# Kernel optimization log

Measured on AMD Instinct MI355X. Metric: run time of the kernel, lower is better.

## Reference

```python
import jax, jax.numpy as jnp
import numpy as np

EMB = 1024
HEADS = 16
HEAD_SZ = EMB // HEADS
EPS = 1e-5


def _layernorm(x, g, b):
    mu = jnp.mean(x, axis=-1, keepdims=True)
    var = jnp.mean(jnp.square(x - mu), axis=-1, keepdims=True)
    return (x - mu) * jax.lax.rsqrt(var + EPS) * g + b


def setup_inputs() -> dict:
    key = jax.random.key(0)
    ks = jax.random.split(key, 12)
    s_in = 1.0 / np.sqrt(EMB)
    s_h = 1.0 / np.sqrt(4 * EMB)
    return {
        "x": jax.random.normal(ks[0], (4, 1024, EMB), jnp.float32),
        # per-head Q/K/V projections stacked: [H, EMB, HEAD_SZ], no bias
        "wq": jax.random.normal(ks[1], (HEADS, EMB, HEAD_SZ), jnp.float32) * s_in,
        "wk": jax.random.normal(ks[2], (HEADS, EMB, HEAD_SZ), jnp.float32) * s_in,
        "wv": jax.random.normal(ks[3], (HEADS, EMB, HEAD_SZ), jnp.float32) * s_in,
        "w_proj": jax.random.normal(ks[4], (EMB, EMB), jnp.float32) * s_in,
        "b_proj": jnp.zeros((EMB,), jnp.float32),
        "w1": jax.random.normal(ks[5], (EMB, 4 * EMB), jnp.float32) * s_in,
        "b1": jnp.zeros((4 * EMB,), jnp.float32),
        "w2": jax.random.normal(ks[6], (4 * EMB, EMB), jnp.float32) * s_h,
        "b2": jnp.zeros((EMB,), jnp.float32),
        "g1": jnp.ones((EMB,), jnp.float32),
        "be1": jnp.zeros((EMB,), jnp.float32),
        "g2": jnp.ones((EMB,), jnp.float32),
        "be2": jnp.zeros((EMB,), jnp.float32),
    }


def reference(x, wq, wk, wv, w_proj, b_proj, w1, b1, w2, b2, g1, be1, g2, be2):
    B, T, C = x.shape
    # --- self-attention (pre-norm) ---
    h = _layernorm(x, g1, be1)
    q = jnp.einsum("btc,hcd->bhtd", h, wq)
    k = jnp.einsum("btc,hcd->bhtd", h, wk)
    v = jnp.einsum("btc,hcd->bhtd", h, wv)
    scale = 1.0 / jnp.sqrt(jnp.asarray(HEAD_SZ, x.dtype))
    scores = jnp.einsum("bhtd,bhsd->bhts", q, k) * scale  # non-causal: SDPA called with no mask
    attn = jax.nn.softmax(scores, axis=-1)
    o = jnp.einsum("bhts,bhsd->bhtd", attn, v)
    o = o.transpose(0, 2, 1, 3).reshape(B, T, C)  # concat heads (same order as torch.cat)
    sa_out = o @ w_proj + b_proj
    x = x + sa_out
    # --- feed-forward; note ln2 applied twice, faithful to source ---
    t = _layernorm(x, g2, be2)
    t = _layernorm(t, g2, be2)
    ff = jax.nn.relu(t @ w1 + b1) @ w2 + b2
    return x + ff
```

## Files before the change

### kernel.cpp

```cpp
#include <hip/hip_runtime.h>
#include <hip/hip_bf16.h>
#include <math.h>
#include <stdint.h>

typedef __bf16 bf16_t;
typedef __bf16 bf16x4 __attribute__((ext_vector_type(4)));
typedef __bf16 bf16x8 __attribute__((ext_vector_type(8)));
typedef float floatx4 __attribute__((ext_vector_type(4)));

#define BM 128
#define BK 32

__device__ __forceinline__ size_t ftaddr(int m, int k, int KT) {
    return ((size_t)(m >> 4) * KT + (k >> 5)) * 512
         + (((k >> 3) & 3) * 16 + (m & 15)) * 8 + (k & 7);
}

__device__ __forceinline__ void gload16(const void* g, void* lds) {
    __builtin_amdgcn_global_load_lds(
        (__attribute__((address_space(1))) void*)(uintptr_t)g,
        (__attribute__((address_space(3))) void*)(uintptr_t)lds,
        16, 0, 0);
}

__global__ void transpose_all(const float* __restrict__ wq, const float* __restrict__ wk,
                              const float* __restrict__ wv, const float* __restrict__ w_proj,
                              const float* __restrict__ w1, const float* __restrict__ w2,
                              bf16_t* __restrict__ WQKVT, bf16_t* __restrict__ WPROJT,
                              bf16_t* __restrict__ W1T, bf16_t* __restrict__ W2T)
{
    const int idx = blockIdx.x;
    const float* in; bf16_t* out; int R, C, rt, ct; long nrow0;
    if (idx < 768) {
        const int z = idx >> 8;
        const int hd = (idx >> 4) & 15;
        rt = idx & 15; ct = 0; R = 1024; C = 64;
        in  = (z == 0 ? wq : z == 1 ? wk : wv) + hd * 65536;
        out = WQKVT; nrow0 = z * 1024 + hd * 64;
    } else if (idx < 1024) {
        const int t = idx - 768; rt = t & 15; ct = t >> 4; R = 1024; C = 1024;
        in = w_proj; out = WPROJT; nrow0 = 0;
    } else if (idx < 2048) {
        const int t = idx - 1024; rt = t & 15; ct = t >> 4; R = 1024; C = 4096;
        in = w1; out = W1T; nrow0 = 0;
    } else {
        const int t = idx - 2048; rt = t & 63; ct = t >> 6; R = 4096; C = 1024;
        in = w2; out = W2T; nrow0 = 0;
    }
    __shared__ float tile[64][65];
    const int tid = threadIdx.x;
    const int r0 = rt * 64, c0 = ct * 64;
    const int tr = tid >> 4;
    const int tc = (tid & 15) * 4;
#pragma unroll
    for (int rr = 0; rr < 4; rr++) {
        const int r = tr + rr * 16;
        const float4 v = *(const float4*)&in[(long)(r0 + r) * C + c0 + tc];
        tile[r][tc + 0] = v.x; tile[r][tc + 1] = v.y;
        tile[r][tc + 2] = v.z; tile[r][tc + 3] = v.w;
    }
    __syncthreads();
    const int KT = R >> 5;
    const int w = tid >> 6, l = tid & 63;
    const int c = l >> 4, rr = l & 15;
#pragma unroll
    for (int it = 0; it < 2; ++it) {
        const int t8 = it * 4 + w;
        const int kt = t8 >> 2;
        const int nb = t8 & 3;
        const long n = nrow0 + c0 + nb * 16 + rr;
        const int k = r0 + kt * 32 + c * 8;
        bf16x8 o;
#pragma unroll
        for (int e = 0; e < 8; e++)
            o[e] = (bf16_t)tile[kt * 32 + c * 8 + e][nb * 16 + rr];
        *(bf16x8*)&out[ftaddr((int)n, k, KT)] = o;
    }
}

__global__ void ln_kernel(const float* __restrict__ x, const float* __restrict__ g,
                          const float* __restrict__ b, bf16_t* __restrict__ outb)
{
    __shared__ __align__(16) bf16_t ybuf[16][1032];
    const int tid = threadIdx.x, wave = tid >> 6, lane = tid & 63;
    const int rb = blockIdx.x;
    float4 gvv[4], bvv[4];
#pragma unroll
    for (int j = 0; j < 4; j++) {
        gvv[j] = ((const float4*)g)[lane + j * 64];
        bvv[j] = ((const float4*)b)[lane + j * 64];
    }
    for (int rr = 0; rr < 4; ++rr) {
        const int lrow = wave * 4 + rr;
        const float* xr = x + (size_t)(rb * 16 + lrow) * 1024;
        float4 v[4];
        float s = 0.f, s2 = 0.f;
#pragma unroll
        for (int j = 0; j < 4; j++) {
            v[j] = ((const float4*)xr)[lane + j * 64];
            s  += v[j].x + v[j].y + v[j].z + v[j].w;
            s2 += v[j].x * v[j].x + v[j].y * v[j].y + v[j].z * v[j].z + v[j].w * v[j].w;
        }
#pragma unroll
        for (int off = 32; off >= 1; off >>= 1) {
            s  += __shfl_xor(s, off);
            s2 += __shfl_xor(s2, off);
        }
        const float mu = s * (1.0f / 1024.0f);
        const float rs = rsqrtf(fmaxf(s2 * (1.0f / 1024.0f) - mu * mu, 0.f) + 1e-5f);
#pragma unroll
        for (int j = 0; j < 4; j++) {
            bf16x4 o;
            o[0] = (bf16_t)((v[j].x - mu) * rs * gvv[j].x + bvv[j].x);
            o[1] = (bf16_t)((v[j].y - mu) * rs * gvv[j].y + bvv[j].y);
            o[2] = (bf16_t)((v[j].z - mu) * rs * gvv[j].z + bvv[j].z);
            o[3] = (bf16_t)((v[j].w - mu) * rs * gvv[j].w + bvv[j].w);
            *(bf16x4*)&ybuf[lrow][(lane + j * 64) * 4] = o;
        }
    }
    __syncthreads();
    bf16_t* outBase = outb + (size_t)rb * 32 * 512;
    for (int it = 0; it < 8; ++it) {
        const int s = it * 256 + tid;
        const int kt = s >> 6, c = (s >> 4) & 3, rr = s & 15;
        const bf16x8 val = *(const bf16x8*)&ybuf[rr][kt * 32 + c * 8];
        *(bf16x8*)&outBase[(size_t)s * 8] = val;
    }
}

__global__ void ln2x_kernel(const float* __restrict__ x, const float* __restrict__ g,
                            const float* __restrict__ b, bf16_t* __restrict__ outb)
{
    __shared__ __align__(16) bf16_t ybuf[16][1032];
    const int tid = threadIdx.x, wave = tid >> 6, lane = tid & 63;
    const int rb = blockIdx.x;
    float4 gvv[4], bvv[4];
#pragma unroll
    for (int j = 0; j < 4; j++) {
        gvv[j] = ((const float4*)g)[lane + j * 64];
        bvv[j] = ((const float4*)b)[lane + j * 64];
    }
    for (int rr = 0; rr < 4; ++rr) {
        const int lrow = wave * 4 + rr;
        const float* xr = x + (size_t)(rb * 16 + lrow) * 1024;
        float4 v[4];
        float s = 0.f, s2 = 0.f;
#pragma unroll
        for (int j = 0; j < 4; j++) {
            v[j] = ((const float4*)xr)[lane + j * 64];
            s  += v[j].x + v[j].y + v[j].z + v[j].w;
            s2 += v[j].x * v[j].x + v[j].y * v[j].y + v[j].z * v[j].z + v[j].w * v[j].w;
        }
#pragma unroll
        for (int off = 32; off >= 1; off >>= 1) {
            s  += __shfl_xor(s, off);
            s2 += __shfl_xor(s2, off);
        }
        float mu = s * (1.0f / 1024.0f);
        float rs = rsqrtf(fmaxf(s2 * (1.0f / 1024.0f) - mu * mu, 0.f) + 1e-5f);
        s = 0.f; s2 = 0.f;
#pragma unroll
        for (int j = 0; j < 4; j++) {
            v[j].x = (v[j].x - mu) * rs * gvv[j].x + bvv[j].x;
            v[j].y = (v[j].y - mu) * rs * gvv[j].y + bvv[j].y;
            v[j].z = (v[j].z - mu) * rs * gvv[j].z + bvv[j].z;
            v[j].w = (v[j].w - mu) * rs * gvv[j].w + bvv[j].w;
            s  += v[j].x + v[j].y + v[j].z + v[j].w;
            s2 += v[j].x * v[j].x + v[j].y * v[j].y + v[j].z * v[j].z + v[j].w * v[j].w;
        }
#pragma unroll
        for (int off = 32; off >= 1; off >>= 1) {
            s  += __shfl_xor(s, off);
            s2 += __shfl_xor(s2, off);
        }
        mu = s * (1.0f / 1024.0f);
        rs = rsqrtf(fmaxf(s2 * (1.0f / 1024.0f) - mu * mu, 0.f) + 1e-5f);
#pragma unroll
        for (int j = 0; j < 4; j++) {
            bf16x4 o;
            o[0] = (bf16_t)((v[j].x - mu) * rs * gvv[j].x + bvv[j].x);
            o[1] = (bf16_t)((v[j].y - mu) * rs * gvv[j].y + bvv[j].y);
            o[2] = (bf16_t)((v[j].z - mu) * rs * gvv[j].z + bvv[j].z);
            o[3] = (bf16_t)((v[j].w - mu) * rs * gvv[j].w + bvv[j].w);
            *(bf16x4*)&ybuf[lrow][(lane + j * 64) * 4] = o;
        }
    }
    __syncthreads();
    bf16_t* outBase = outb + (size_t)rb * 32 * 512;
    for (int it = 0; it < 8; ++it) {
        const int s = it * 256 + tid;
        const int kt = s >> 6, c = (s >> 4) & 3, rr = s & 15;
        const bf16x8 val = *(const bf16x8*)&ybuf[rr][kt * 32 + c * 8];
        *(bf16x8*)&outBase[(size_t)s * 8] = val;
    }
}

template<int EPI, int BNt>
__global__ __launch_bounds__(256, 2)
void gemm_bt(const bf16_t* __restrict__ A, const bf16_t* __restrict__ Bt,
             const int K,
             const float* __restrict__ bias, const float* __restrict__ resid,
             float* __restrict__ outf, bf16_t* __restrict__ outb,
             bf16_t* __restrict__ aux1, bf16_t* __restrict__ aux2,
             const int Nout)
{
    constexpr int NFRAG = BNt / 16;
    __shared__ __align__(16) bf16_t As[3][8 * 512];
    __shared__ __align__(16) bf16_t Bs[3][NFRAG * 512];
    const int tid  = threadIdx.x;
    const int wave = tid >> 6, lane = tid & 63;
    const int bm = blockIdx.x * BM, bn = blockIdx.y * BNt;
    const int KT = K >> 5;

    floatx4 acc[2][NFRAG];
#pragma unroll
    for (int i = 0; i < 2; i++)
#pragma unroll
        for (int j = 0; j < NFRAG; j++) acc[i][j] = (floatx4){0.f, 0.f, 0.f, 0.f};

    const bf16_t* gA0 = A + ((size_t)(bm / 16 + wave * 2 + 0) * KT) * 512 + lane * 8;
    const bf16_t* gA1 = A + ((size_t)(bm / 16 + wave * 2 + 1) * KT) * 512 + lane * 8;
    const int lA0 = (wave * 2 + 0) * 512;
    const int lA1 = (wave * 2 + 1) * 512;

    const bf16_t* gB0;
    const bf16_t* gB1 = nullptr;
    int lB0, lB1 = 0;
    if (BNt == 128) {
        gB0 = Bt + ((size_t)(bn / 16 + wave * 2 + 0) * KT) * 512 + lane * 8;
        gB1 = Bt + ((size_t)(bn / 16 + wave * 2 + 1) * KT) * 512 + lane * 8;
        lB0 = (wave * 2 + 0) * 512;
        lB1 = (wave * 2 + 1) * 512;
    } else {
        gB0 = Bt + ((size_t)(bn / 16 + wave) * KT) * 512 + lane * 8;
        lB0 = wave * 512;
    }

    auto stage = [&](int t, int bu) {
        const size_t off = (size_t)t * 512;
        gload16(gA0 + off, (bf16_t*)As[bu] + lA0);
        gload16(gA1 + off, (bf16_t*)As[bu] + lA1);
        gload16(gB0 + off, (bf16_t*)Bs[bu] + lB0);
        if (BNt == 128) gload16(gB1 + off, (bf16_t*)Bs[bu] + lB1);
    };

    auto compute = [&](int bu) {
        bf16x8 af[2], bfv[NFRAG];
#pragma unroll
        for (int i = 0; i < 2; i++)
            af[i] = *(const bf16x8*)&As[bu][(wave * 2 + i) * 512 + lane * 8];
#pragma unroll
        for (int j = 0; j < NFRAG; j++)
            bfv[j] = *(const bf16x8*)&Bs[bu][j * 512 + lane * 8];
#pragma unroll
        for (int i = 0; i < 2; i++)
#pragma unroll
            for (int j = 0; j < NFRAG; j++)
                acc[i][j] = __builtin_amdgcn_mfma_f32_16x16x32_bf16(af[i], bfv[j], acc[i][j], 0, 0, 0);
    };

    const int NT = K / BK;
    stage(0, 0);
    stage(1, 1);
    int bu = 0;
    for (int t = 0; t < NT - 1; ++t) {
        if (BNt == 128) asm volatile("s_waitcnt vmcnt(4)\n\ts_barrier" ::: "memory");
        else            asm volatile("s_waitcnt vmcnt(3)\n\ts_barrier" ::: "memory");
        if (t + 2 < NT) stage(t + 2, (t + 2) % 3);
        compute(bu);
        bu = (bu + 1) % 3;
    }
    asm volatile("s_waitcnt vmcnt(0)\n\ts_barrier" ::: "memory");
    compute(bu);

    const int er = (lane >> 4) * 4, ec = lane & 15;
#pragma unroll
    for (int i = 0; i < 2; i++) {
#pragma unroll
        for (int j = 0; j < NFRAG; j++) {
            const int col = bn + j * 16 + ec;
#pragma unroll
            for (int r = 0; r < 4; r++) {
                const int row = bm + wave * 32 + i * 16 + er + r;
                const float v = acc[i][j][r];
                if (EPI == 0) {
                    const int b = row >> 10, t = row & 1023;
                    if (col < 1024) {
                        const int h = col >> 6, d = col & 63;
                        outb[(size_t)((b * 16 + h) * 1024 + t) * 64 + d] = (bf16_t)v;
                    } else if (col < 2048) {
                        const int c2 = col - 1024, h = c2 >> 6, d = c2 & 63;
                        aux1[(size_t)((b * 16 + h) * 1024 + t) * 64 + d] = (bf16_t)v;
                    } else {
                        const int c2 = col - 2048, h = c2 >> 6, d = c2 & 63;
                        aux2[(size_t)((b * 16 + h) * 64 + d) * 1024 + t] = (bf16_t)v;
                    }
                } else if (EPI == 1 || EPI == 3) {
                    const size_t idx = (size_t)row * Nout + col;
                    outf[idx] = v + bias[col] + resid[idx];
                } else if (EPI == 2) {
                    outb[ftaddr(row, col, Nout >> 5)] = (bf16_t)fmaxf(v + bias[col], 0.f);
                }
            }
        }
    }
}

__global__ __launch_bounds__(256, 4)
void attn_kernel(const bf16_t* __restrict__ Q, const bf16_t* __restrict__ Kg,
                 const bf16_t* __restrict__ Vt, bf16_t* __restrict__ Og)
{
    __shared__ __align__(16) bf16_t Ks[2][4096];
    __shared__ __align__(16) bf16_t Vs[2][4096];
    __shared__ __align__(16) bf16_t Ps[4][1024];
    const int tid = threadIdx.x, wave = tid >> 6, lane = tid & 63;
    const int bh = blockIdx.y;
    const int b = bh >> 4, h = bh & 15;
    const int q0 = blockIdx.x * 64 + wave * 16;
    const bf16_t* Qb = Q + (size_t)bh * 65536;
    const char* Kb = (const char*)(Kg + (size_t)bh * 65536);
    const char* Vb = (const char*)(Vt + (size_t)bh * 65536);
    const int fr = lane & 15, g = lane >> 4, fk = g * 8;

    const bf16x8 qf0 = *(const bf16x8*)&Qb[(size_t)(q0 + fr) * 64 + fk];
    const bf16x8 qf1 = *(const bf16x8*)&Qb[(size_t)(q0 + fr) * 64 + 32 + fk];

    floatx4 o[4];
#pragma unroll
    for (int dt = 0; dt < 4; dt++) o[dt] = (floatx4){0.f, 0.f, 0.f, 0.f};
    float lsum[4] = {0.f, 0.f, 0.f, 0.f};
    bf16_t* pw = &Ps[wave][0];
    const float sscale = 0.125f * 1.44269504088896f;

    auto stage = [&](int s0, int bu) {
#pragma unroll
        for (int t = 0; t < 2; t++) {
            const int j = wave * 2 + t;
            gload16(Kb + (size_t)(s0 + lane) * 128 + j * 16, &Ks[bu][j * 512]);
            gload16(Vb + (size_t)lane * 2048 + (size_t)s0 * 2 + j * 16, &Vs[bu][j * 512]);
        }
    };

    stage(0, 0);
    int bu = 0;
    for (int it = 0; it < 16; ++it) {
        __syncthreads();
        if (it < 15) stage((it + 1) * 64, bu ^ 1);
        const bf16_t* Kl = Ks[bu];
        const bf16_t* Vl = Vs[bu];

        floatx4 sacc[4];
#pragma unroll
        for (int ss = 0; ss < 4; ss++) sacc[ss] = (floatx4){0.f, 0.f, 0.f, 0.f};
#pragma unroll
        for (int c = 0; c < 2; c++) {
            const int ch = c * 4 + g;
            const bf16x8 qf = (c == 0) ? qf0 : qf1;
#pragma unroll
            for (int ss = 0; ss < 4; ss++) {
                const bf16x8 kf = *(const bf16x8*)&Kl[ch * 512 + (ss * 16 + fr) * 8];
                sacc[ss] = __builtin_amdgcn_mfma_f32_16x16x32_bf16(qf, kf, sacc[ss], 0, 0, 0);
            }
        }
#pragma unroll
        for (int ss = 0; ss < 4; ss++) {
#pragma unroll
            for (int r = 0; r < 4; r++) {
                const float p = __builtin_amdgcn_exp2f(sacc[ss][r] * sscale);
                lsum[r] += p;
                const int q = g * 4 + r;
                pw[(ss * 2 + (fr >> 3)) * 128 + q * 8 + (fr & 7)] = (bf16_t)p;
            }
        }
        asm volatile("s_waitcnt lgkmcnt(0)" ::: "memory");
#pragma unroll
        for (int c = 0; c < 2; c++) {
            const int ch = c * 4 + g;
            const bf16x8 pf = *(const bf16x8*)&pw[ch * 128 + fr * 8];
#pragma unroll
            for (int dt = 0; dt < 4; dt++) {
                const bf16x8 vf = *(const bf16x8*)&Vl[ch * 512 + (dt * 16 + fr) * 8];
                o[dt] = __builtin_amdgcn_mfma_f32_16x16x32_bf16(pf, vf, o[dt], 0, 0, 0);
            }
        }
        asm volatile("" ::: "memory");
        bu ^= 1;
    }
#pragma unroll
    for (int r = 0; r < 4; r++) {
        float l = lsum[r];
        l += __shfl_xor(l, 1);
        l += __shfl_xor(l, 2);
        l += __shfl_xor(l, 4);
        l += __shfl_xor(l, 8);
        lsum[r] = 1.0f / l;
    }
    const int tq = q0 + g * 4;
#pragma unroll
    for (int dt = 0; dt < 4; dt++) {
#pragma unroll
        for (int r = 0; r < 4; r++) {
            const int m = b * 1024 + tq + r;
            const int k = h * 64 + dt * 16 + fr;
            Og[ftaddr(m, k, 32)] = (bf16_t)(o[dt][r] * lsum[r]);
        }
    }
}

extern "C" void kernel_launch(void* const* d_in, const int* in_sizes, int n_in,
                              void* d_out, int out_size, void* d_ws, size_t ws_size,
                              hipStream_t stream)
{
    const float* x      = (const float*)d_in[0];
    const float* wq     = (const float*)d_in[1];
    const float* wk     = (const float*)d_in[2];
    const float* wv     = (const float*)d_in[3];
    const float* w_proj = (const float*)d_in[4];
    const float* b_proj = (const float*)d_in[5];
    const float* w1     = (const float*)d_in[6];
    const float* b1     = (const float*)d_in[7];
    const float* w2     = (const float*)d_in[8];
    const float* b2     = (const float*)d_in[9];
    const float* g1     = (const float*)d_in[10];
    const float* be1    = (const float*)d_in[11];
    const float* g2     = (const float*)d_in[12];
    const float* be2    = (const float*)d_in[13];
    float* out = (float*)d_out;
    char* ws = (char*)d_ws;

    bf16_t* WQKVT = (bf16_t*)(ws + 0x0000000);
    bf16_t* WPROJT= (bf16_t*)(ws + 0x0600000);
    bf16_t* W1T   = (bf16_t*)(ws + 0x0800000);
    bf16_t* W2T   = (bf16_t*)(ws + 0x1000000);
    bf16_t* HB    = (bf16_t*)(ws + 0x1800000);
    bf16_t* Qb    = (bf16_t*)(ws + 0x2000000);
    bf16_t* Kb    = (bf16_t*)(ws + 0x2800000);
    bf16_t* Vtb   = (bf16_t*)(ws + 0x3000000);
    bf16_t* AO    = (bf16_t*)(ws + 0x3800000);
    float*  X2    = (float*)(ws + 0x4000000);
    bf16_t* TB    = (bf16_t*)(ws + 0x2800000);
    bf16_t* FF1B  = (bf16_t*)(ws + 0x5000000);

    dim3 blk(256);
    transpose_all<<<3072, blk, 0, stream>>>(wq, wk, wv, w_proj, w1, w2,
                                            WQKVT, WPROJT, W1T, W2T);
    ln_kernel<<<256, blk, 0, stream>>>(x, g1, be1, HB);
    gemm_bt<0, 128><<<dim3(32, 24), blk, 0, stream>>>(HB, WQKVT, 1024, nullptr, nullptr,
                                                      nullptr, Qb, Kb, Vtb, 3072);
    attn_kernel<<<dim3(16, 64), blk, 0, stream>>>(Qb, Kb, Vtb, AO);
    gemm_bt<1, 64><<<dim3(32, 16), blk, 0, stream>>>(AO, WPROJT, 1024, b_proj, x,
                                                     X2, nullptr, nullptr, nullptr, 1024);
    ln2x_kernel<<<256, blk, 0, stream>>>(X2, g2, be2, TB);
    gemm_bt<2, 128><<<dim3(32, 32), blk, 0, stream>>>(TB, W1T, 1024, b1, nullptr,
                                                      nullptr, FF1B, nullptr, nullptr, 4096);
    gemm_bt<3, 64><<<dim3(32, 16), blk, 0, stream>>>(FF1B, W2T, 4096, b2, X2,
                                                     out, nullptr, nullptr, nullptr, 1024);
}
```

Measured before the change: 316.8 us.

## Merge weight transpose with LN1 and stage V-transpose epilogue through LDS

```diff
diff --git a/kernel.cpp b/kernel.cpp
--- a/kernel.cpp
+++ b/kernel.cpp
@@ -23,63 +23,116 @@
         16, 0, 0);
 }
 
-__global__ void transpose_all(const float* __restrict__ wq, const float* __restrict__ wk,
-                              const float* __restrict__ wv, const float* __restrict__ w_proj,
-                              const float* __restrict__ w1, const float* __restrict__ w2,
-                              bf16_t* __restrict__ WQKVT, bf16_t* __restrict__ WPROJT,
-                              bf16_t* __restrict__ W1T, bf16_t* __restrict__ W2T)
+__global__ void prep_kernel(const float* __restrict__ wq, const float* __restrict__ wk,
+                            const float* __restrict__ wv, const float* __restrict__ w_proj,
+                            const float* __restrict__ w1, const float* __restrict__ w2,
+                            bf16_t* __restrict__ WQKVT, bf16_t* __restrict__ WPROJT,
+                            bf16_t* __restrict__ W1T, bf16_t* __restrict__ W2T,
+                            const float* __restrict__ x, const float* __restrict__ g1,
+                            const float* __restrict__ be1, bf16_t* __restrict__ HB)
 {
-    const int idx = blockIdx.x;
-    const float* in; bf16_t* out; int R, C, rt, ct; long nrow0;
-    if (idx < 768) {
-        const int z = idx >> 8;
-        const int hd = (idx >> 4) & 15;
-        rt = idx & 15; ct = 0; R = 1024; C = 64;
-        in  = (z == 0 ? wq : z == 1 ? wk : wv) + hd * 65536;
-        out = WQKVT; nrow0 = z * 1024 + hd * 64;
-    } else if (idx < 1024) {
-        const int t = idx - 768; rt = t & 15; ct = t >> 4; R = 1024; C = 1024;
-        in = w_proj; out = WPROJT; nrow0 = 0;
-    } else if (idx < 2048) {
-        const int t = idx - 1024; rt = t & 15; ct = t >> 4; R = 1024; C = 4096;
-        in = w1; out = W1T; nrow0 = 0;
+    __shared__ __align__(16) char psm[33024];
+    const int tid = threadIdx.x;
+    if (blockIdx.x < 3072) {
+        float (*tile)[65] = (float(*)[65])psm;
+        const int idx = blockIdx.x;
+        const float* in; bf16_t* out; int R, C, rt, ct; long nrow0;
+        if (idx < 768) {
+            const int z = idx >> 8;
+            const int hd = (idx >> 4) & 15;
+            rt = idx & 15; ct = 0; R = 1024; C = 64;
+            in  = (z == 0 ? wq : z == 1 ? wk : wv) + hd * 65536;
+            out = WQKVT; nrow0 = z * 1024 + hd * 64;
+        } else if (idx < 1024) {
+            const int t = idx - 768; rt = t & 15; ct = t >> 4; R = 1024; C = 1024;
+            in = w_proj; out = WPROJT; nrow0 = 0;
+        } else if (idx < 2048) {
+            const int t = idx - 1024; rt = t & 15; ct = t >> 4; R = 1024; C = 4096;
+            in = w1; out = W1T; nrow0 = 0;
+        } else {
+            const int t = idx - 2048; rt = t & 63; ct = t >> 6; R = 4096; C = 1024;
+            in = w2; out = W2T; nrow0 = 0;
+        }
+        const int r0 = rt * 64, c0 = ct * 64;
+        const int tr = tid >> 4;
+        const int tc = (tid & 15) * 4;
+#pragma unroll
+        for (int rr = 0; rr < 4; rr++) {
+            const int r = tr + rr * 16;
+            const float4 v = *(const float4*)&in[(long)(r0 + r) * C + c0 + tc];
+            tile[r][tc + 0] = v.x; tile[r][tc + 1] = v.y;
+            tile[r][tc + 2] = v.z; tile[r][tc + 3] = v.w;
+        }
+        __syncthreads();
+        const int KT = R >> 5;
+        const int w = tid >> 6, l = tid & 63;
+        const int c = l >> 4, rr2 = l & 15;
+#pragma unroll
+        for (int it = 0; it < 2; ++it) {
+            const int t8 = it * 4 + w;
+            const int kt = t8 >> 2;
+            const int nb = t8 & 3;
+            const long n = nrow0 + c0 + nb * 16 + rr2;
+            const int k = r0 + kt * 32 + c * 8;
+            bf16x8 o;
+#pragma unroll
+            for (int e = 0; e < 8; e++)
+                o[e] = (bf16_t)tile[kt * 32 + c * 8 + e][nb * 16 + rr2];
+            *(bf16x8*)&out[ftaddr((int)n, k, KT)] = o;
+        }
     } else {
-        const int t = idx - 2048; rt = t & 63; ct = t >> 6; R = 4096; C = 1024;
-        in = w2; out = W2T; nrow0 = 0;
-    }
-    __shared__ float tile[64][65];
-    const int tid = threadIdx.x;
-    const int r0 = rt * 64, c0 = ct * 64;
-    const int tr = tid >> 4;
-    const int tc = (tid & 15) * 4;
-#pragma unroll
-    for (int rr = 0; rr < 4; rr++) {
-        const int r = tr + rr * 16;
-        const float4 v = *(const float4*)&in[(long)(r0 + r) * C + c0 + tc];
-        tile[r][tc + 0] = v.x; tile[r][tc + 1] = v.y;
-        tile[r][tc + 2] = v.z; tile[r][tc + 3] = v.w;
-    }
-    __syncthreads();
-    const int KT = R >> 5;
-    const int w = tid >> 6, l = tid & 63;
-    const int c = l >> 4, rr = l & 15;
-#pragma unroll
-    for (int it = 0; it < 2; ++it) {
-        const int t8 = it * 4 + w;
-        const int kt = t8 >> 2;
-        const int nb = t8 & 3;
-        const long n = nrow0 + c0 + nb * 16 + rr;
-        const int k = r0 + kt * 32 + c * 8;
-        bf16x8 o;
-#pragma unroll
-        for (int e = 0; e < 8; e++)
-            o[e] = (bf16_t)tile[kt * 32 + c * 8 + e][nb * 16 + rr];
-        *(bf16x8*)&out[ftaddr((int)n, k, KT)] = o;
-    }
-}
-
-__global__ void ln_kernel(const float* __restrict__ x, const float* __restrict__ g,
-                          const float* __restrict__ b, bf16_t* __restrict__ outb)
+        bf16_t (*ybuf)[1032] = (bf16_t(*)[1032])psm;
+        const int wave = tid >> 6, lane = tid & 63;
+        const int rb = blockIdx.x - 3072;
+        float4 gvv[4], bvv[4];
+#pragma unroll
+        for (int j = 0; j < 4; j++) {
+            gvv[j] = ((const float4*)g1)[lane + j * 64];
+            bvv[j] = ((const float4*)be1)[lane + j * 64];
+        }
+#pragma unroll
+        for (int rr = 0; rr < 4; ++rr) {
+            const int lrow = wave * 4 + rr;
+            const float* xr = x + (size_t)(rb * 16 + lrow) * 1024;
+            float4 v[4];
+            float s = 0.f, s2 = 0.f;
+#pragma unroll
+            for (int j = 0; j < 4; j++) {
+                v[j] = ((const float4*)xr)[lane + j * 64];
+                s  += v[j].x + v[j].y + v[j].z + v[j].w;
+                s2 += v[j].x * v[j].x + v[j].y * v[j].y + v[j].z * v[j].z + v[j].w * v[j].w;
+            }
+#pragma unroll
+            for (int off = 32; off >= 1; off >>= 1) {
+                s  += __shfl_xor(s, off);
+                s2 += __shfl_xor(s2, off);
+            }
+            const float mu = s * (1.0f / 1024.0f);
+            const float rs = rsqrtf(fmaxf(s2 * (1.0f / 1024.0f) - mu * mu, 0.f) + 1e-5f);
+#pragma unroll
+            for (int j = 0; j < 4; j++) {
+                bf16x4 o;
+                o[0] = (bf16_t)((v[j].x - mu) * rs * gvv[j].x + bvv[j].x);
+                o[1] = (bf16_t)((v[j].y - mu) * rs * gvv[j].y + bvv[j].y);
+                o[2] = (bf16_t)((v[j].z - mu) * rs * gvv[j].z + bvv[j].z);
+                o[3] = (bf16_t)((v[j].w - mu) * rs * gvv[j].w + bvv[j].w);
+                *(bf16x4*)&ybuf[lrow][(lane + j * 64) * 4] = o;
+            }
+        }
+        __syncthreads();
+        bf16_t* outBase = HB + (size_t)rb * 32 * 512;
+#pragma unroll
+        for (int it = 0; it < 8; ++it) {
+            const int s = it * 256 + tid;
+            const int kt = s >> 6, c = (s >> 4) & 3, rr2 = s & 15;
+            const bf16x8 val = *(const bf16x8*)&ybuf[rr2][kt * 32 + c * 8];
+            *(bf16x8*)&outBase[(size_t)s * 8] = val;
+        }
+    }
+}
+
+__global__ void ln2x_kernel(const float* __restrict__ x, const float* __restrict__ g,
+                            const float* __restrict__ b, bf16_t* __restrict__ outb)
 {
     __shared__ __align__(16) bf16_t ybuf[16][1032];
     const int tid = threadIdx.x, wave = tid >> 6, lane = tid & 63;
@@ -90,6 +143,7 @@
         gvv[j] = ((const float4*)g)[lane + j * 64];
         bvv[j] = ((const float4*)b)[lane + j * 64];
     }
+#pragma unroll
     for (int rr = 0; rr < 4; ++rr) {
         const int lrow = wave * 4 + rr;
         const float* xr = x + (size_t)(rb * 16 + lrow) * 1024;
@@ -106,8 +160,25 @@
             s  += __shfl_xor(s, off);
             s2 += __shfl_xor(s2, off);
         }
-        const float mu = s * (1.0f / 1024.0f);
-        const float rs = rsqrtf(fmaxf(s2 * (1.0f / 1024.0f) - mu * mu, 0.f) + 1e-5f);
+        float mu = s * (1.0f / 1024.0f);
+        float rs = rsqrtf(fmaxf(s2 * (1.0f / 1024.0f) - mu * mu, 0.f) + 1e-5f);
+        s = 0.f; s2 = 0.f;
+#pragma unroll
+        for (int j = 0; j < 4; j++) {
+            v[j].x = (v[j].x - mu) * rs * gvv[j].x + bvv[j].x;
+            v[j].y = (v[j].y - mu) * rs * gvv[j].y + bvv[j].y;
+            v[j].z = (v[j].z - mu) * rs * gvv[j].z + bvv[j].z;
+            v[j].w = (v[j].w - mu) * rs * gvv[j].w + bvv[j].w;
+            s  += v[j].x + v[j].y + v[j].z + v[j].w;
+            s2 += v[j].x * v[j].x + v[j].y * v[j].y + v[j].z * v[j].z + v[j].w * v[j].w;
+        }
+#pragma unroll
+        for (int off = 32; off >= 1; off >>= 1) {
+            s  += __shfl_xor(s, off);
+            s2 += __shfl_xor(s2, off);
+        }
+        mu = s * (1.0f / 1024.0f);
+        rs = rsqrtf(fmaxf(s2 * (1.0f / 1024.0f) - mu * mu, 0.f) + 1e-5f);
 #pragma unroll
         for (int j = 0; j < 4; j++) {
             bf16x4 o;
@@ -120,77 +191,11 @@
     }
     __syncthreads();
     bf16_t* outBase = outb + (size_t)rb * 32 * 512;
+#pragma unroll
     for (int it = 0; it < 8; ++it) {
         const int s = it * 256 + tid;
-        const int kt = s >> 6, c = (s >> 4) & 3, rr = s & 15;
-        const bf16x8 val = *(const bf16x8*)&ybuf[rr][kt * 32 + c * 8];
-        *(bf16x8*)&outBase[(size_t)s * 8] = val;
-    }
-}
-
-__global__ void ln2x_kernel(const float* __restrict__ x, const float* __restrict__ g,
-                            const float* __restrict__ b, bf16_t* __restrict__ outb)
-{
-    __shared__ __align__(16) bf16_t ybuf[16][1032];
-    const int tid = threadIdx.x, wave = tid >> 6, lane = tid & 63;
-    const int rb = blockIdx.x;
-    float4 gvv[4], bvv[4];
-#pragma unroll
-    for (int j = 0; j < 4; j++) {
-        gvv[j] = ((const float4*)g)[lane + j * 64];
-        bvv[j] = ((const float4*)b)[lane + j * 64];
-    }
-    for (int rr = 0; rr < 4; ++rr) {
-        const int lrow = wave * 4 + rr;
-        const float* xr = x + (size_t)(rb * 16 + lrow) * 1024;
-        float4 v[4];
-        float s = 0.f, s2 = 0.f;
-#pragma unroll
-        for (int j = 0; j < 4; j++) {
-            v[j] = ((const float4*)xr)[lane + j * 64];
-            s  += v[j].x + v[j].y + v[j].z + v[j].w;
-            s2 += v[j].x * v[j].x + v[j].y * v[j].y + v[j].z * v[j].z + v[j].w * v[j].w;
-        }
-#pragma unroll
-        for (int off = 32; off >= 1; off >>= 1) {
-            s  += __shfl_xor(s, off);
-            s2 += __shfl_xor(s2, off);
-        }
-        float mu = s * (1.0f / 1024.0f);
-        float rs = rsqrtf(fmaxf(s2 * (1.0f / 1024.0f) - mu * mu, 0.f) + 1e-5f);
-        s = 0.f; s2 = 0.f;
-#pragma unroll
-        for (int j = 0; j < 4; j++) {
-            v[j].x = (v[j].x - mu) * rs * gvv[j].x + bvv[j].x;
-            v[j].y = (v[j].y - mu) * rs * gvv[j].y + bvv[j].y;
-            v[j].z = (v[j].z - mu) * rs * gvv[j].z + bvv[j].z;
-            v[j].w = (v[j].w - mu) * rs * gvv[j].w + bvv[j].w;
-            s  += v[j].x + v[j].y + v[j].z + v[j].w;
-            s2 += v[j].x * v[j].x + v[j].y * v[j].y + v[j].z * v[j].z + v[j].w * v[j].w;
-        }
-#pragma unroll
-        for (int off = 32; off >= 1; off >>= 1) {
-            s  += __shfl_xor(s, off);
-            s2 += __shfl_xor(s2, off);
-        }
-        mu = s * (1.0f / 1024.0f);
-        rs = rsqrtf(fmaxf(s2 * (1.0f / 1024.0f) - mu * mu, 0.f) + 1e-5f);
-#pragma unroll
-        for (int j = 0; j < 4; j++) {
-            bf16x4 o;
-            o[0] = (bf16_t)((v[j].x - mu) * rs * gvv[j].x + bvv[j].x);
-            o[1] = (bf16_t)((v[j].y - mu) * rs * gvv[j].y + bvv[j].y);
-            o[2] = (bf16_t)((v[j].z - mu) * rs * gvv[j].z + bvv[j].z);
-            o[3] = (bf16_t)((v[j].w - mu) * rs * gvv[j].w + bvv[j].w);
-            *(bf16x4*)&ybuf[lrow][(lane + j * 64) * 4] = o;
-        }
-    }
-    __syncthreads();
-    bf16_t* outBase = outb + (size_t)rb * 32 * 512;
-    for (int it = 0; it < 8; ++it) {
-        const int s = it * 256 + tid;
-        const int kt = s >> 6, c = (s >> 4) & 3, rr = s & 15;
-        const bf16x8 val = *(const bf16x8*)&ybuf[rr][kt * 32 + c * 8];
+        const int kt = s >> 6, c = (s >> 4) & 3, rr2 = s & 15;
+        const bf16x8 val = *(const bf16x8*)&ybuf[rr2][kt * 32 + c * 8];
         *(bf16x8*)&outBase[(size_t)s * 8] = val;
     }
 }
@@ -205,8 +210,11 @@
              const int Nout)
 {
     constexpr int NFRAG = BNt / 16;
-    __shared__ __align__(16) bf16_t As[3][8 * 512];
-    __shared__ __align__(16) bf16_t Bs[3][NFRAG * 512];
+    constexpr int ASZ = 3 * 8 * 512;
+    constexpr int BSZ = 3 * NFRAG * 512;
+    __shared__ __align__(16) bf16_t smem[ASZ + BSZ];
+    bf16_t* Asb = smem;
+    bf16_t* Bsb = smem + ASZ;
     const int tid  = threadIdx.x;
     const int wave = tid >> 6, lane = tid & 63;
     const int bm = blockIdx.x * BM, bn = blockIdx.y * BNt;
@@ -238,20 +246,20 @@
 
     auto stage = [&](int t, int bu) {
         const size_t off = (size_t)t * 512;
-        gload16(gA0 + off, (bf16_t*)As[bu] + lA0);
-        gload16(gA1 + off, (bf16_t*)As[bu] + lA1);
-        gload16(gB0 + off, (bf16_t*)Bs[bu] + lB0);
-        if (BNt == 128) gload16(gB1 + off, (bf16_t*)Bs[bu] + lB1);
+        gload16(gA0 + off, Asb + bu * 4096 + lA0);
+        gload16(gA1 + off, Asb + bu * 4096 + lA1);
+        gload16(gB0 + off, Bsb + bu * (NFRAG * 512) + lB0);
+        if (BNt == 128) gload16(gB1 + off, Bsb + bu * (NFRAG * 512) + lB1);
     };
 
     auto compute = [&](int bu) {
         bf16x8 af[2], bfv[NFRAG];
 #pragma unroll
         for (int i = 0; i < 2; i++)
-            af[i] = *(const bf16x8*)&As[bu][(wave * 2 + i) * 512 + lane * 8];
+            af[i] = *(const bf16x8*)&Asb[bu * 4096 + (wave * 2 + i) * 512 + lane * 8];
 #pragma unroll
         for (int j = 0; j < NFRAG; j++)
-            bfv[j] = *(const bf16x8*)&Bs[bu][j * 512 + lane * 8];
+            bfv[j] = *(const bf16x8*)&Bsb[bu * (NFRAG * 512) + j * 512 + lane * 8];
 #pragma unroll
         for (int i = 0; i < 2; i++)
 #pragma unroll
@@ -274,6 +282,29 @@
     compute(bu);
 
     const int er = (lane >> 4) * 4, ec = lane & 15;
+    if (EPI == 0 && bn >= 2048) {
+        __syncthreads();
+        bf16_t* scr = smem;
+#pragma unroll
+        for (int i = 0; i < 2; i++)
+#pragma unroll
+            for (int j = 0; j < NFRAG; j++)
+#pragma unroll
+                for (int r = 0; r < 4; r++)
+                    scr[(j * 16 + ec) * 136 + wave * 32 + i * 16 + er + r] =
+                        (bf16_t)acc[i][j][r];
+        __syncthreads();
+        const int bq = bm >> 10, tmod = bm & 1023, h0 = (bn - 2048) >> 6;
+#pragma unroll
+        for (int it = 0; it < 8; ++it) {
+            const int c = it * 256 + tid;
+            const int dl = c >> 4, t16 = c & 15;
+            const bf16x8 val = *(const bf16x8*)&scr[dl * 136 + t16 * 8];
+            const int h = h0 + (dl >> 6), dd = dl & 63;
+            *(bf16x8*)&aux2[(size_t)((bq * 16 + h) * 64 + dd) * 1024 + tmod + t16 * 8] = val;
+        }
+        return;
+    }
 #pragma unroll
     for (int i = 0; i < 2; i++) {
 #pragma unroll
@@ -288,12 +319,9 @@
                     if (col < 1024) {
                         const int h = col >> 6, d = col & 63;
                         outb[(size_t)((b * 16 + h) * 1024 + t) * 64 + d] = (bf16_t)v;
-                    } else if (col < 2048) {
+                    } else {
                         const int c2 = col - 1024, h = c2 >> 6, d = c2 & 63;
                         aux1[(size_t)((b * 16 + h) * 1024 + t) * 64 + d] = (bf16_t)v;
-                    } else {
-                        const int c2 = col - 2048, h = c2 >> 6, d = c2 & 63;
-                        aux2[(size_t)((b * 16 + h) * 64 + d) * 1024 + t] = (bf16_t)v;
                     }
                 } else if (EPI == 1 || EPI == 3) {
                     const size_t idx = (size_t)row * Nout + col;
@@ -442,9 +470,9 @@
     bf16_t* FF1B  = (bf16_t*)(ws + 0x5000000);
 
     dim3 blk(256);
-    transpose_all<<<3072, blk, 0, stream>>>(wq, wk, wv, w_proj, w1, w2,
-                                            WQKVT, WPROJT, W1T, W2T);
-    ln_kernel<<<256, blk, 0, stream>>>(x, g1, be1, HB);
+    prep_kernel<<<3328, blk, 0, stream>>>(wq, wk, wv, w_proj, w1, w2,
+                                          WQKVT, WPROJT, W1T, W2T,
+                                          x, g1, be1, HB);
     gemm_bt<0, 128><<<dim3(32, 24), blk, 0, stream>>>(HB, WQKVT, 1024, nullptr, nullptr,
                                                       nullptr, Qb, Kb, Vtb, 3072);
     attn_kernel<<<dim3(16, 64), blk, 0, stream>>>(Qb, Kb, Vtb, AO);
```

New measurement: 297.5 us. 1.06x faster.
